# Kernel tuning notes

Hardware: AMD Instinct MI355X
Metric: run time of the kernel (lower is better)

The kernel has to match this reference:

```python
import jax, jax.numpy as jnp
import numpy as np

WINDOW_SIZES = (2, 4, 8)
HIDDEN = 32


def setup_inputs() -> dict:
    key = jax.random.key(0)
    ks = jax.random.split(key, 8)
    B, H, L = 4, 16, 1024
    S = len(WINDOW_SIZES)
    inp = {
        "attn_1": jax.random.uniform(ks[0], (B, H, L, L), dtype=jnp.float32),
        "attn_2": jax.random.uniform(ks[1], (B, H, L, L), dtype=jnp.float32),
        # gate MLP params, stacked over scales: Linear(8->32), Linear(32->16), Linear(16->1)
        "W1": jax.random.normal(ks[2], (S, HIDDEN, 8), dtype=jnp.float32) * 0.2,
        "b1": jnp.zeros((S, HIDDEN), dtype=jnp.float32),
        "W2": jax.random.normal(ks[3], (S, HIDDEN // 2, HIDDEN), dtype=jnp.float32) * 0.2,
        "b2": jnp.zeros((S, HIDDEN // 2), dtype=jnp.float32),
        "W3": jax.random.normal(ks[4], (S, 1, HIDDEN // 2), dtype=jnp.float32) * 0.2,
        "b3": jnp.zeros((S, 1), dtype=jnp.float32),
        "scale_weights": jnp.ones((S,), dtype=jnp.float32) / S,
    }
    return inp


def _window_stats(attn, ws):
    # attn: [B,H,L,L]; L % ws == 0 -> all windows are full-size (no edge merge)
    B, H, L, _ = attn.shape
    nw = L // ws
    x = attn.reshape(B, H, nw, ws, L)
    mean = x.mean(axis=-1).mean(axis=-1)                 # [B,H,nw]
    std = jnp.std(x, axis=-1, ddof=1).mean(axis=-1)      # torch.std is unbiased
    mx = x.max(axis=-1).mean(axis=-1)
    mn = x.min(axis=-1).mean(axis=-1)
    return jnp.stack([mean, std, mx, mn], axis=-1)        # [B,H,nw,4]


def reference(attn_1, attn_2, W1, b1, W2, b2, W3, b3, scale_weights):
    B, H, L, _ = attn_1.shape
    alphas = []
    for s, ws in enumerate(WINDOW_SIZES):
        g = jnp.concatenate([_window_stats(attn_1, ws), _window_stats(attn_2, ws)], axis=-1)  # [B,H,nw,8]
        h = jax.nn.relu(jnp.einsum('bhnf,of->bhno', g, W1[s]) + b1[s])
        h = jax.nn.relu(jnp.einsum('bhnf,of->bhno', h, W2[s]) + b2[s])
        a = jax.nn.sigmoid(jnp.einsum('bhnf,of->bhno', h, W3[s]) + b3[s])  # [B,H,nw,1]
        # expand per-window alpha to per-frame: repeat ws times (nw*ws == L)
        a_exp = jnp.repeat(a[..., 0], ws, axis=-1)[..., None]  # [B,H,L,1]
        alphas.append(a_exp)
    w = jax.nn.softmax(scale_weights)                     # all scales valid (max ws <= L)
    alpha_stacked = jnp.stack(alphas, axis=-1)            # [B,H,L,1,S]
    alpha_final = (alpha_stacked * w.reshape(1, 1, 1, 1, -1)).sum(axis=-1)
    return alpha_final
```

## Files before the change

### kernel.cpp

```cpp
#include <hip/hip_runtime.h>
#include <math.h>

#define L_DIM 1024
#define BH 64
#define ROWS_PER_TENSOR (BH * L_DIM)

typedef float floatx4 __attribute__((ext_vector_type(4)));

__global__ __launch_bounds__(256) void row_stats_kernel(
    const float* __restrict__ a1, const float* __restrict__ a2,
    float4* __restrict__ stats)
{
    const int wave = (blockIdx.x << 2) | (threadIdx.x >> 6);
    const int lane = threadIdx.x & 63;
    const int t = wave >> 16;
    const int r = wave & (ROWS_PER_TENSOR - 1);
    const float* __restrict__ src = t ? a2 : a1;
    const floatx4* __restrict__ rowp = (const floatx4*)(src + (size_t)r * L_DIM);

    float s = 0.f, sq = 0.f, mx = -INFINITY, mn = INFINITY;
#pragma unroll
    for (int c = 0; c < 4; ++c) {
        floatx4 v = __builtin_nontemporal_load(&rowp[(c << 6) + lane]);
        s  += v.x + v.y + v.z + v.w;
        sq += v.x * v.x + v.y * v.y + v.z * v.z + v.w * v.w;
        mx = fmaxf(mx, fmaxf(fmaxf(v.x, v.y), fmaxf(v.z, v.w)));
        mn = fminf(mn, fminf(fminf(v.x, v.y), fminf(v.z, v.w)));
    }
#pragma unroll
    for (int off = 32; off > 0; off >>= 1) {
        s  += __shfl_xor(s,  off, 64);
        sq += __shfl_xor(sq, off, 64);
        mx = fmaxf(mx, __shfl_xor(mx, off, 64));
        mn = fminf(mn, __shfl_xor(mn, off, 64));
    }
    if (lane == 0) {
        const float invL = 1.0f / (float)L_DIM;
        float mean = s * invL;
        float var  = (sq - s * s * invL) * (1.0f / (float)(L_DIM - 1));
        var = fmaxf(var, 0.f);
        float4 o;
        o.x = mean; o.y = sqrtf(var); o.z = mx; o.w = mn;
        stats[wave] = o;
    }
}

__global__ __launch_bounds__(256) void gate_kernel(
    const float4* __restrict__ stats,
    const float* __restrict__ W1, const float* __restrict__ b1,
    const float* __restrict__ W2, const float* __restrict__ b2,
    const float* __restrict__ W3, const float* __restrict__ b3,
    const float* __restrict__ sw,
    float* __restrict__ out)
{
    __shared__ float alpha[224];

    const int bh = blockIdx.x >> 2;
    const int l0 = (blockIdx.x & 3) << 8;
    const int tid = threadIdx.x;

    const float4* __restrict__ st1 = stats + (size_t)bh * L_DIM;
    const float4* __restrict__ st2 = stats + ROWS_PER_TENSOR + (size_t)bh * L_DIM;

    if (tid < 224) {
        int s, ws, r0;
        if (tid < 128)      { s = 0; ws = 2; r0 = l0 + (tid << 1); }
        else if (tid < 192) { s = 1; ws = 4; r0 = l0 + ((tid - 128) << 2); }
        else                { s = 2; ws = 8; r0 = l0 + ((tid - 192) << 3); }

        const int su = __builtin_amdgcn_readfirstlane(s);
        const float* __restrict__ W1p = W1 + su * 256;
        const float* __restrict__ b1p = b1 + su * 32;
        const float* __restrict__ W2p = W2 + su * 512;
        const float* __restrict__ b2p = b2 + su * 16;
        const float* __restrict__ W3p = W3 + su * 16;
        const float  b3v = b3[su];

        float g[8] = {0.f, 0.f, 0.f, 0.f, 0.f, 0.f, 0.f, 0.f};
        for (int j = 0; j < ws; ++j) {
            float4 v1 = st1[r0 + j];
            float4 v2 = st2[r0 + j];
            g[0] += v1.x; g[1] += v1.y; g[2] += v1.z; g[3] += v1.w;
            g[4] += v2.x; g[5] += v2.y; g[6] += v2.z; g[7] += v2.w;
        }
        const float inv = 1.0f / (float)ws;
#pragma unroll
        for (int k = 0; k < 8; ++k) g[k] *= inv;

        float h1[32];
#pragma unroll
        for (int o = 0; o < 32; ++o) {
            float acc = b1p[o];
#pragma unroll
            for (int f = 0; f < 8; ++f) acc += W1p[o * 8 + f] * g[f];
            h1[o] = fmaxf(acc, 0.f);
        }
        float h2[16];
#pragma unroll
        for (int o = 0; o < 16; ++o) {
            float acc = b2p[o];
#pragma unroll
            for (int f = 0; f < 32; ++f) acc += W2p[o * 32 + f] * h1[f];
            h2[o] = fmaxf(acc, 0.f);
        }
        float acc = b3v;
#pragma unroll
        for (int f = 0; f < 16; ++f) acc += W3p[f] * h2[f];

        alpha[tid] = 1.0f / (1.0f + expf(-acc));
    }
    __syncthreads();

    const float s0 = sw[0], s1 = sw[1], s2 = sw[2];
    const float m = fmaxf(s0, fmaxf(s1, s2));
    const float e0 = expf(s0 - m), e1 = expf(s1 - m), e2 = expf(s2 - m);
    const float einv = 1.0f / (e0 + e1 + e2);
    const float w0 = e0 * einv, w1 = e1 * einv, w2 = e2 * einv;

    out[(size_t)bh * L_DIM + l0 + tid] =
          w0 * alpha[tid >> 1]
        + w1 * alpha[128 + (tid >> 2)]
        + w2 * alpha[192 + (tid >> 3)];
}

extern "C" void kernel_launch(void* const* d_in, const int* in_sizes, int n_in,
                              void* d_out, int out_size, void* d_ws, size_t ws_size,
                              hipStream_t stream) {
    const float* attn1 = (const float*)d_in[0];
    const float* attn2 = (const float*)d_in[1];
    const float* W1 = (const float*)d_in[2];
    const float* b1 = (const float*)d_in[3];
    const float* W2 = (const float*)d_in[4];
    const float* b2 = (const float*)d_in[5];
    const float* W3 = (const float*)d_in[6];
    const float* b3 = (const float*)d_in[7];
    const float* sw = (const float*)d_in[8];
    float* out = (float*)d_out;

    float4* stats = (float4*)d_ws;

    const int n_rows = 2 * ROWS_PER_TENSOR;
    row_stats_kernel<<<n_rows / 4, 256, 0, stream>>>(attn1, attn2, stats);

    gate_kernel<<<BH * 4, 256, 0, stream>>>(stats, W1, b1, W2, b2, W3, b3, sw, out);
}
```

Before: 495.6 us.

## Fuse row statistics and gate MLP into a single kernel

Merges the row-stats pass and the gate MLP pass into one kernel. Each 512-thread block handles 8 rows of both attention tensors, keeps their stats in shared memory, and runs the three per-scale MLPs on a few lanes before writing 8 outputs. This drops the workspace round trip and the second launch. In exchange, the MLP runs serialized on one or a few lanes per block after a barrier, which could stall memory streaming if occupancy cannot hide it.

```diff
diff --git a/kernel.cpp b/kernel.cpp
--- a/kernel.cpp
+++ b/kernel.cpp
@@ -3,124 +3,132 @@
 
 #define L_DIM 1024
 #define BH 64
-#define ROWS_PER_TENSOR (BH * L_DIM)
+#define ROWS (BH * L_DIM)
 
 typedef float floatx4 __attribute__((ext_vector_type(4)));
 
-__global__ __launch_bounds__(256) void row_stats_kernel(
-    const float* __restrict__ a1, const float* __restrict__ a2,
-    float4* __restrict__ stats)
+
+template <int S, int WS>
+__device__ __forceinline__ void run_mlp(
+    const float (*sm)[8], int base,
+    const float* __restrict__ W1, const float* __restrict__ b1,
+    const float* __restrict__ W2, const float* __restrict__ b2,
+    const float* __restrict__ W3, const float* __restrict__ b3,
+    float* dst)
 {
-    const int wave = (blockIdx.x << 2) | (threadIdx.x >> 6);
-    const int lane = threadIdx.x & 63;
-    const int t = wave >> 16;
-    const int r = wave & (ROWS_PER_TENSOR - 1);
-    const float* __restrict__ src = t ? a2 : a1;
-    const floatx4* __restrict__ rowp = (const floatx4*)(src + (size_t)r * L_DIM);
+    const float* __restrict__ W1p = W1 + S * 256;
+    const float* __restrict__ b1p = b1 + S * 32;
+    const float* __restrict__ W2p = W2 + S * 512;
+    const float* __restrict__ b2p = b2 + S * 16;
+    const float* __restrict__ W3p = W3 + S * 16;
+    const float  b3v = b3[S];
 
-    float s = 0.f, sq = 0.f, mx = -INFINITY, mn = INFINITY;
+    float g[8] = {0.f, 0.f, 0.f, 0.f, 0.f, 0.f, 0.f, 0.f};
 #pragma unroll
-    for (int c = 0; c < 4; ++c) {
-        floatx4 v = __builtin_nontemporal_load(&rowp[(c << 6) + lane]);
-        s  += v.x + v.y + v.z + v.w;
-        sq += v.x * v.x + v.y * v.y + v.z * v.z + v.w * v.w;
-        mx = fmaxf(mx, fmaxf(fmaxf(v.x, v.y), fmaxf(v.z, v.w)));
-        mn = fminf(mn, fminf(fminf(v.x, v.y), fminf(v.z, v.w)));
+    for (int j = 0; j < WS; ++j)
+#pragma unroll
+        for (int k = 0; k < 8; ++k) g[k] += sm[base + j][k];
+    const float inv = 1.0f / (float)WS;
+#pragma unroll
+    for (int k = 0; k < 8; ++k) g[k] *= inv;
+
+    float h1[32];
+#pragma unroll
+    for (int o = 0; o < 32; ++o) {
+        float acc = b1p[o];
+#pragma unroll
+        for (int f = 0; f < 8; ++f) acc += W1p[o * 8 + f] * g[f];
+        h1[o] = fmaxf(acc, 0.f);
     }
+    float h2[16];
 #pragma unroll
-    for (int off = 32; off > 0; off >>= 1) {
-        s  += __shfl_xor(s,  off, 64);
-        sq += __shfl_xor(sq, off, 64);
-        mx = fmaxf(mx, __shfl_xor(mx, off, 64));
-        mn = fminf(mn, __shfl_xor(mn, off, 64));
+    for (int o = 0; o < 16; ++o) {
+        float acc = b2p[o];
+#pragma unroll
+        for (int f = 0; f < 32; ++f) acc += W2p[o * 32 + f] * h1[f];
+        h2[o] = fmaxf(acc, 0.f);
     }
-    if (lane == 0) {
-        const float invL = 1.0f / (float)L_DIM;
-        float mean = s * invL;
-        float var  = (sq - s * s * invL) * (1.0f / (float)(L_DIM - 1));
-        var = fmaxf(var, 0.f);
-        float4 o;
-        o.x = mean; o.y = sqrtf(var); o.z = mx; o.w = mn;
-        stats[wave] = o;
-    }
+    float acc = b3v;
+#pragma unroll
+    for (int f = 0; f < 16; ++f) acc += W3p[f] * h2[f];
+
+    *dst = 1.0f / (1.0f + expf(-acc));
 }
 
-__global__ __launch_bounds__(256) void gate_kernel(
-    const float4* __restrict__ stats,
+__global__ __launch_bounds__(512) void fused_gate_kernel(
+    const float* __restrict__ a1, const float* __restrict__ a2,
     const float* __restrict__ W1, const float* __restrict__ b1,
     const float* __restrict__ W2, const float* __restrict__ b2,
     const float* __restrict__ W3, const float* __restrict__ b3,
     const float* __restrict__ sw,
     float* __restrict__ out)
 {
-    __shared__ float alpha[224];
+    __shared__ float sm[8][8];
+    __shared__ float aw[8];
 
-    const int bh = blockIdx.x >> 2;
-    const int l0 = (blockIdx.x & 3) << 8;
-    const int tid = threadIdx.x;
+    const int wave = threadIdx.x >> 6;
+    const int lane = threadIdx.x & 63;
+    const int r = (blockIdx.x << 3) | wave;
 
-    const float4* __restrict__ st1 = stats + (size_t)bh * L_DIM;
-    const float4* __restrict__ st2 = stats + ROWS_PER_TENSOR + (size_t)bh * L_DIM;
+    const floatx4* __restrict__ r1 = (const floatx4*)(a1 + (size_t)r * L_DIM);
+    const floatx4* __restrict__ r2 = (const floatx4*)(a2 + (size_t)r * L_DIM);
 
-    if (tid < 224) {
-        int s, ws, r0;
-        if (tid < 128)      { s = 0; ws = 2; r0 = l0 + (tid << 1); }
-        else if (tid < 192) { s = 1; ws = 4; r0 = l0 + ((tid - 128) << 2); }
-        else                { s = 2; ws = 8; r0 = l0 + ((tid - 192) << 3); }
-
-        const int su = __builtin_amdgcn_readfirstlane(s);
-        const float* __restrict__ W1p = W1 + su * 256;
-        const float* __restrict__ b1p = b1 + su * 32;
-        const float* __restrict__ W2p = W2 + su * 512;
-        const float* __restrict__ b2p = b2 + su * 16;
-        const float* __restrict__ W3p = W3 + su * 16;
-        const float  b3v = b3[su];
-
-        float g[8] = {0.f, 0.f, 0.f, 0.f, 0.f, 0.f, 0.f, 0.f};
-        for (int j = 0; j < ws; ++j) {
-            float4 v1 = st1[r0 + j];
-            float4 v2 = st2[r0 + j];
-            g[0] += v1.x; g[1] += v1.y; g[2] += v1.z; g[3] += v1.w;
-            g[4] += v2.x; g[5] += v2.y; g[6] += v2.z; g[7] += v2.w;
-        }
-        const float inv = 1.0f / (float)ws;
+    float s1 = 0.f, q1 = 0.f, mx1 = -INFINITY, mn1 = INFINITY;
+    float s2 = 0.f, q2 = 0.f, mx2 = -INFINITY, mn2 = INFINITY;
 #pragma unroll
-        for (int k = 0; k < 8; ++k) g[k] *= inv;
-
-        float h1[32];
+    for (int c = 0; c < 4; ++c) {
+        floatx4 v = __builtin_nontemporal_load(&r1[(c << 6) + lane]);
+        floatx4 u = __builtin_nontemporal_load(&r2[(c << 6) + lane]);
+        s1 += v.x + v.y + v.z + v.w;
+        q1 += v.x * v.x + v.y * v.y + v.z * v.z + v.w * v.w;
+        mx1 = fmaxf(mx1, fmaxf(fmaxf(v.x, v.y), fmaxf(v.z, v.w)));
+        mn1 = fminf(mn1, fminf(fminf(v.x, v.y), fminf(v.z, v.w)));
+        s2 += u.x + u.y + u.z + u.w;
+        q2 += u.x * u.x + u.y * u.y + u.z * u.z + u.w * u.w;
+        mx2 = fmaxf(mx2, fmaxf(fmaxf(u.x, u.y), fmaxf(u.z, u.w)));
+        mn2 = fminf(mn2, fminf(fminf(u.x, u.y), fminf(u.z, u.w)));
+    }
 #pragma unroll
-        for (int o = 0; o < 32; ++o) {
-            float acc = b1p[o];
-#pragma unroll
-            for (int f = 0; f < 8; ++f) acc += W1p[o * 8 + f] * g[f];
-            h1[o] = fmaxf(acc, 0.f);
-        }
-        float h2[16];
-#pragma unroll
-        for (int o = 0; o < 16; ++o) {
-            float acc = b2p[o];
-#pragma unroll
-            for (int f = 0; f < 32; ++f) acc += W2p[o * 32 + f] * h1[f];
-            h2[o] = fmaxf(acc, 0.f);
-        }
-        float acc = b3v;
-#pragma unroll
-        for (int f = 0; f < 16; ++f) acc += W3p[f] * h2[f];
-
-        alpha[tid] = 1.0f / (1.0f + expf(-acc));
+    for (int off = 32; off > 0; off >>= 1) {
+        s1 += __shfl_xor(s1, off, 64);
+        q1 += __shfl_xor(q1, off, 64);
+        mx1 = fmaxf(mx1, __shfl_xor(mx1, off, 64));
+        mn1 = fminf(mn1, __shfl_xor(mn1, off, 64));
+        s2 += __shfl_xor(s2, off, 64);
+        q2 += __shfl_xor(q2, off, 64);
+        mx2 = fmaxf(mx2, __shfl_xor(mx2, off, 64));
+        mn2 = fminf(mn2, __shfl_xor(mn2, off, 64));
+    }
+    if (lane == 0) {
+        const float invL = 1.0f / (float)L_DIM;
+        const float invN = 1.0f / (float)(L_DIM - 1);
+        float m1 = s1 * invL, m2 = s2 * invL;
+        float v1 = fmaxf((q1 - s1 * s1 * invL) * invN, 0.f);
+        float v2 = fmaxf((q2 - s2 * s2 * invL) * invN, 0.f);
+        sm[wave][0] = m1; sm[wave][1] = sqrtf(v1); sm[wave][2] = mx1; sm[wave][3] = mn1;
+        sm[wave][4] = m2; sm[wave][5] = sqrtf(v2); sm[wave][6] = mx2; sm[wave][7] = mn2;
     }
     __syncthreads();
 
-    const float s0 = sw[0], s1 = sw[1], s2 = sw[2];
-    const float m = fmaxf(s0, fmaxf(s1, s2));
-    const float e0 = expf(s0 - m), e1 = expf(s1 - m), e2 = expf(s2 - m);
-    const float einv = 1.0f / (e0 + e1 + e2);
-    const float w0 = e0 * einv, w1 = e1 * einv, w2 = e2 * einv;
+    if (wave == 0) {
+        if (lane < 4) run_mlp<0, 2>(sm, lane << 1, W1, b1, W2, b2, W3, b3, &aw[lane]);
+    } else if (wave == 1) {
+        if (lane < 2) run_mlp<1, 4>(sm, lane << 2, W1, b1, W2, b2, W3, b3, &aw[4 + lane]);
+    } else if (wave == 2) {
+        if (lane == 0) run_mlp<2, 8>(sm, 0, W1, b1, W2, b2, W3, b3, &aw[6]);
+    }
+    __syncthreads();
 
-    out[(size_t)bh * L_DIM + l0 + tid] =
-          w0 * alpha[tid >> 1]
-        + w1 * alpha[128 + (tid >> 2)]
-        + w2 * alpha[192 + (tid >> 3)];
+    if (threadIdx.x < 8) {
+        const float t0 = sw[0], t1 = sw[1], t2 = sw[2];
+        const float m = fmaxf(t0, fmaxf(t1, t2));
+        const float e0 = expf(t0 - m), e1 = expf(t1 - m), e2 = expf(t2 - m);
+        const float einv = 1.0f / (e0 + e1 + e2);
+        out[(blockIdx.x << 3) + threadIdx.x] =
+              (e0 * einv) * aw[threadIdx.x >> 1]
+            + (e1 * einv) * aw[4 + (threadIdx.x >> 2)]
+            + (e2 * einv) * aw[6];
+    }
 }
 
 extern "C" void kernel_launch(void* const* d_in, const int* in_sizes, int n_in,
@@ -137,10 +145,6 @@
     const float* sw = (const float*)d_in[8];
     float* out = (float*)d_out;
 
-    float4* stats = (float4*)d_ws;
-
-    const int n_rows = 2 * ROWS_PER_TENSOR;
-    row_stats_kernel<<<n_rows / 4, 256, 0, stream>>>(attn1, attn2, stats);
-
-    gate_kernel<<<BH * 4, 256, 0, stream>>>(stats, W1, b1, W2, b2, W3, b3, sw, out);
+    fused_gate_kernel<<<ROWS / 8, 512, 0, stream>>>(
+        attn1, attn2, W1, b1, W2, b2, W3, b3, sw, out);
 }
```

Result: no change. 499.0 us (+0.7%).
